# Performance work log

Hardware: AMD Instinct MI355X
Metric: run time of the kernel (lower is better)

Reference implementation:

```python
import jax, jax.numpy as jnp
import numpy as np

B, N, E, H, FF = 8, 1024, 512, 8, 2048
D = E // H
SCALE = D ** -0.5
EPS = 1e-5


def _layernorm(x, g, b):
    mu = jnp.mean(x, axis=-1, keepdims=True)
    var = jnp.mean((x - mu) ** 2, axis=-1, keepdims=True)
    return (x - mu) * jax.lax.rsqrt(var + EPS) * g + b


def setup_inputs() -> dict:
    key = jax.random.key(0)
    ks = jax.random.split(key, 16)
    s = lambda fan_in: 1.0 / np.sqrt(fan_in)
    inp = {"x": jax.random.normal(ks[0], (B, N, E), jnp.float32)}
    # attention projections, stored as [in, out] so y = x @ W + b
    inp["Wq"] = jax.random.uniform(ks[1], (E, E), jnp.float32, -s(E), s(E))
    inp["bq"] = jnp.zeros((E,), jnp.float32)
    inp["Wk"] = jax.random.uniform(ks[2], (E, E), jnp.float32, -s(E), s(E))
    inp["bk"] = jnp.zeros((E,), jnp.float32)
    inp["Wv"] = jax.random.uniform(ks[3], (E, E), jnp.float32, -s(E), s(E))
    inp["bv"] = jnp.zeros((E,), jnp.float32)
    inp["Wo"] = jax.random.uniform(ks[4], (E, E), jnp.float32, -s(E), s(E))
    inp["bo"] = jnp.zeros((E,), jnp.float32)
    # layernorms
    inp["g1"] = jnp.ones((E,), jnp.float32)
    inp["b1"] = jnp.zeros((E,), jnp.float32)
    inp["g2"] = jnp.ones((E,), jnp.float32)
    inp["b2"] = jnp.zeros((E,), jnp.float32)
    # feed-forward
    inp["W1"] = jax.random.uniform(ks[5], (E, FF), jnp.float32, -s(E), s(E))
    inp["bf1"] = jnp.zeros((FF,), jnp.float32)
    inp["W2"] = jax.random.uniform(ks[6], (FF, E), jnp.float32, -s(FF), s(FF))
    inp["bf2"] = jnp.zeros((E,), jnp.float32)
    return inp


def reference(x, Wq, bq, Wk, bk, Wv, bv, Wo, bo, g1, b1, g2, b2, W1, bf1, W2, bf2):
    # --- multi-head self-attention (equivalent to the edge scatter-softmax:
    # softmax over all source nodes j for each target node i) ---
    q = (x @ Wq + bq).reshape(B, N, H, D)
    k = (x @ Wk + bk).reshape(B, N, H, D)
    v = (x @ Wv + bv).reshape(B, N, H, D)
    scores = jnp.einsum("bnhd,bmhd->bhnm", q, k) * SCALE  # [B,H,N,N]
    attn = jax.nn.softmax(scores, axis=-1)
    ctx = jnp.einsum("bhnm,bmhd->bnhd", attn, v).reshape(B, N, E)
    attn_out = ctx @ Wo + bo
    # --- residual + norm1 ---
    h1 = _layernorm(x + attn_out, g1, b1)
    # --- FFN: linear -> relu -> linear ---
    ffn = jax.nn.relu(h1 @ W1 + bf1) @ W2 + bf2
    # --- residual + norm2 ---
    return _layernorm(h1 + ffn, g2, b2)
```

## Files before the change

kernel.cpp:

```cpp
#include <hip/hip_runtime.h>
#include <cstdint>
#include <cstddef>

typedef unsigned short u16;
typedef __attribute__((ext_vector_type(8))) short bf16x8;
typedef __attribute__((ext_vector_type(4))) float f32x4;
typedef __attribute__((ext_vector_type(16))) float f32x16;

#define EPI_F32 0
#define EPI_BF16_RELU 1
#define EPI_QKV 2
#define EPI_PART 3

#define QSCALE 0.18033688011112042f

__device__ __forceinline__ u16 f2bf(float f) {
  uint32_t u = __float_as_uint(f);
  return (u16)((u + 0x7FFFu + ((u >> 16) & 1u)) >> 16);
}

__device__ __forceinline__ uint32_t cvt_pk_bf16(float lo, float hi) {
  uint32_t r;
  asm("v_cvt_pk_bf16_f32 %0, %1, %2" : "=v"(r) : "v"(lo), "v"(hi));
  return r;
}

__device__ __forceinline__ float fexp2(float x) { return __builtin_amdgcn_exp2f(x); }

__device__ __forceinline__ void gload_lds16(const void* g, void* l) {
  __builtin_amdgcn_global_load_lds((const __attribute__((address_space(1))) void*)g,
                                   (__attribute__((address_space(3))) void*)l, 16, 0, 0);
}

__device__ __forceinline__ void tcvt_tile(const float* __restrict__ W,
                                          u16* __restrict__ Wt, int K, int N,
                                          int bx, int by, float (*tl)[33], int t) {
  const int kr0 = by * 32, nc0 = bx * 32;
  const int r = t >> 3, cq = (t & 7) * 4;
  float4 v = *(const float4*)&W[(size_t)(kr0 + r) * N + nc0 + cq];
  tl[r][cq + 0] = v.x; tl[r][cq + 1] = v.y; tl[r][cq + 2] = v.z; tl[r][cq + 3] = v.w;
  __syncthreads();
  union { u16 u[4]; uint2 q; } pk;
#pragma unroll
  for (int j = 0; j < 4; ++j) pk.u[j] = f2bf(tl[cq + j][r]);
  *(uint2*)&Wt[(size_t)(nc0 + r) * K + kr0 + cq] = pk.q;
}

__global__ __launch_bounds__(256) void prep_kernel(
    const float* __restrict__ x, u16* __restrict__ xb,
    const float* __restrict__ Wq, const float* __restrict__ Wk,
    const float* __restrict__ Wv, const float* __restrict__ Wo,
    u16* __restrict__ Wqkvt, u16* __restrict__ Wot,
    const float* __restrict__ W1, u16* __restrict__ W1t,
    const float* __restrict__ W2, u16* __restrict__ W2t,
    const float* __restrict__ bq, const float* __restrict__ bk,
    const float* __restrict__ bv, float* __restrict__ bqkv) {
  __shared__ float tl[32][33];
  const int b = blockIdx.x, t = threadIdx.x;
  if (b < 2048) {
    const int i = b * 256 + t;
    const float4* p = (const float4*)x + (size_t)i * 2;
    float4 a = p[0], c = p[1];
    union { u16 u[8]; uint4 q; } pk;
    pk.u[0] = f2bf(a.x); pk.u[1] = f2bf(a.y); pk.u[2] = f2bf(a.z); pk.u[3] = f2bf(a.w);
    pk.u[4] = f2bf(c.x); pk.u[5] = f2bf(c.y); pk.u[6] = f2bf(c.z); pk.u[7] = f2bf(c.w);
    ((uint4*)xb)[i] = pk.q;
  } else if (b < 3072) {
    const int u = b - 2048, z = u >> 8, s = u & 255;
    const float* W = z == 0 ? Wq : (z == 1 ? Wk : (z == 2 ? Wv : Wo));
    u16* Wt = z < 3 ? Wqkvt + z * 262144 : Wot;
    tcvt_tile(W, Wt, 512, 512, s & 15, s >> 4, tl, t);
  } else if (b < 4096) {
    const int u = b - 3072;
    tcvt_tile(W1, W1t, 512, 2048, u % 64, u / 64, tl, t);
  } else if (b < 5120) {
    const int u = b - 4096;
    tcvt_tile(W2, W2t, 2048, 512, u % 16, u / 16, tl, t);
  } else {
    const int i = (b - 5120) * 256 + t;
    if (i < 1536) bqkv[i] = i < 512 ? bq[i] : (i < 1024 ? bk[i - 512] : bv[i - 1024]);
  }
}

template<int BM, int BN, int WM, int WN, int EPI, int SPLIT>
__global__ __launch_bounds__(256, 2) void gemm2_kernel(
    const u16* __restrict__ A, const u16* __restrict__ Bt,
    const float* __restrict__ bias, void* __restrict__ out,
    int M, int N, int K) {
  constexpr int NWN = BN / WN;
  constexpr int MI = WM / 16, NI = WN / 16;
  __shared__ u16 As[2][BM * 64];
  __shared__ u16 Bs[2][BN * 64];
  const int tid = threadIdx.x, lane = tid & 63, wave = tid >> 6;
  const int m0 = blockIdx.y * BM, n0 = blockIdx.x * BN;
  const int wm = wave / NWN, wn = wave % NWN;
  const int g = lane >> 4, lr = lane & 15;
  const int srow = tid >> 3, sslot = tid & 7;

#define STAGE2(buf, k0) do {                                                        \
    _Pragma("unroll")                                                               \
    for (int i_ = 0; i_ < BM / 32; ++i_) {                                          \
      const int r_ = i_ * 32 + srow;                                                \
      gload_lds16(A + (size_t)(m0 + r_) * K + (k0) + ((sslot ^ (r_ & 7)) << 3),     \
                  &As[buf][i_ * 2048 + tid * 8]);                                   \
    }                                                                               \
    _Pragma("unroll")                                                               \
    for (int i_ = 0; i_ < BN / 32; ++i_) {                                          \
      const int r_ = i_ * 32 + srow;                                                \
      gload_lds16(Bt + (size_t)(n0 + r_) * K + (k0) + ((sslot ^ (r_ & 7)) << 3),    \
                  &Bs[buf][i_ * 2048 + tid * 8]);                                   \
    }                                                                               \
  } while (0)

  f32x4 acc[MI][NI] = {};
  const int kBeg = (SPLIT > 1) ? blockIdx.z * (K / SPLIT) : 0;
  const int NT = ((SPLIT > 1) ? K / SPLIT : K) >> 6;

  STAGE2(0, kBeg);
  STAGE2(1, kBeg + 64);
  asm volatile("s_waitcnt vmcnt(8)" ::: "memory");
  __builtin_amdgcn_s_barrier();
  asm volatile("" ::: "memory");

  for (int t = 0; t < NT; ++t) {
    const int cur = t & 1;
    bf16x8 af[MI][2], bf[NI][2];
#pragma unroll
    for (int step = 0; step < 2; ++step) {
#pragma unroll
      for (int mi = 0; mi < MI; ++mi) {
        const int r = wm * WM + mi * 16 + lr;
        af[mi][step] = *(const bf16x8*)&As[cur][r * 64 + ((((step << 2) + g) ^ (r & 7)) << 3)];
      }
#pragma unroll
      for (int ni = 0; ni < NI; ++ni) {
        const int r = wn * WN + ni * 16 + lr;
        bf[ni][step] = *(const bf16x8*)&Bs[cur][r * 64 + ((((step << 2) + g) ^ (r & 7)) << 3)];
      }
    }
    __builtin_amdgcn_s_setprio(1);
#pragma unroll
    for (int step = 0; step < 2; ++step)
#pragma unroll
      for (int mi = 0; mi < MI; ++mi)
#pragma unroll
        for (int ni = 0; ni < NI; ++ni)
          acc[mi][ni] = __builtin_amdgcn_mfma_f32_16x16x32_bf16(af[mi][step], bf[ni][step],
                                                                acc[mi][ni], 0, 0, 0);
    __builtin_amdgcn_s_setprio(0);
    asm volatile("s_waitcnt lgkmcnt(0)" ::: "memory");
    __builtin_amdgcn_sched_barrier(0);
    __builtin_amdgcn_s_barrier();
    asm volatile("" ::: "memory");
    if (t + 2 < NT) {
      STAGE2(cur, kBeg + (t + 2) * 64);
      asm volatile("s_waitcnt vmcnt(8)" ::: "memory");
    } else {
      asm volatile("s_waitcnt vmcnt(0)" ::: "memory");
    }
    __builtin_amdgcn_s_barrier();
    asm volatile("" ::: "memory");
  }
#undef STAGE2

#pragma unroll
  for (int mi = 0; mi < MI; ++mi) {
#pragma unroll
    for (int ni = 0; ni < NI; ++ni) {
      const int col = n0 + wn * WN + ni * 16 + lr;
      const float bv = (EPI == EPI_PART) ? 0.f : bias[col];
      f32x4 v = acc[mi][ni];
#pragma unroll
      for (int r = 0; r < 4; ++r) {
        const int row = m0 + wm * WM + mi * 16 + g * 4 + r;
        const float y = v[r] + bv;
        if (EPI == EPI_F32) {
          ((float*)out)[(size_t)row * N + col] = y;
        } else if (EPI == EPI_PART) {
          ((float*)out)[(size_t)blockIdx.z * M * N + (size_t)row * N + col] = y;
        } else if (EPI == EPI_BF16_RELU) {
          ((u16*)out)[(size_t)row * N + col] = f2bf(fmaxf(y, 0.f));
        } else {
          u16* qb = (u16*)out;
          const int sec = col >> 9, cs = col & 511;
          const int b = row >> 10, tt = row & 1023, h = cs >> 6, d = cs & 63;
          if (sec == 0)
            qb[((size_t)((b * 8 + h) * 1024 + tt)) * 64 + d] = f2bf(y * QSCALE);
          else if (sec == 1)
            qb[4194304 + ((size_t)((b * 8 + h) * 1024 + tt)) * 64 + d] = f2bf(y);
          else
            qb[8388608 + ((size_t)((b * 8 + h) * 64 + d)) * 1024 + tt] = f2bf(y);
        }
      }
    }
  }
}

template<int BM, int BN, int WM, int WN, int EPI, int SPLIT>
__global__ __launch_bounds__(256) void gemm_kernel(
    const u16* __restrict__ A, const u16* __restrict__ Bt,
    const float* __restrict__ bias, void* __restrict__ out,
    int M, int N, int K) {
  constexpr int NWN = BN / WN;
  constexpr int MI = WM / 16, NI = WN / 16;
  __shared__ u16 As[BM * 32];
  __shared__ u16 Bs[BN * 32];
  const int tid = threadIdx.x;
  const int lane = tid & 63;
  const int wave = tid >> 6;
  const int m0 = blockIdx.y * BM;
  const int n0 = blockIdx.x * BN;
  const int wm = wave / NWN, wn = wave % NWN;
  const int g = lane >> 4, lr = lane & 15;
  const int srow = lane >> 2, scol = (lane & 3) * 8;

  f32x4 acc[MI][NI] = {};

  const int kBeg = (SPLIT > 1) ? blockIdx.z * (K / SPLIT) : 0;
  const int kEnd = (SPLIT > 1) ? kBeg + (K / SPLIT) : K;
  for (int k0 = kBeg; k0 < kEnd; k0 += 32) {
#pragma unroll
    for (int ch = wave; ch < BM / 16; ch += 4)
      gload_lds16(A + (size_t)(m0 + ch * 16 + srow) * K + k0 + scol, &As[ch * 512]);
#pragma unroll
    for (int ch = wave; ch < BN / 16; ch += 4)
      gload_lds16(Bt + (size_t)(n0 + ch * 16 + srow) * K + k0 + scol, &Bs[ch * 512]);
    __syncthreads();
    bf16x8 a[MI], b[NI];
#pragma unroll
    for (int mi = 0; mi < MI; ++mi) a[mi] = *(const bf16x8*)&As[(wm * WM + mi * 16 + lr) * 32 + g * 8];
#pragma unroll
    for (int ni = 0; ni < NI; ++ni) b[ni] = *(const bf16x8*)&Bs[(wn * WN + ni * 16 + lr) * 32 + g * 8];
#pragma unroll
    for (int mi = 0; mi < MI; ++mi)
#pragma unroll
      for (int ni = 0; ni < NI; ++ni)
        acc[mi][ni] = __builtin_amdgcn_mfma_f32_16x16x32_bf16(a[mi], b[ni], acc[mi][ni], 0, 0, 0);
    __syncthreads();
  }

#pragma unroll
  for (int mi = 0; mi < MI; ++mi) {
#pragma unroll
    for (int ni = 0; ni < NI; ++ni) {
      const int col = n0 + wn * WN + ni * 16 + lr;
      const float bv = (EPI == EPI_PART) ? 0.f : bias[col];
      f32x4 v = acc[mi][ni];
#pragma unroll
      for (int r = 0; r < 4; ++r) {
        const int row = m0 + wm * WM + mi * 16 + g * 4 + r;
        const float y = v[r] + bv;
        if (EPI == EPI_F32) {
          ((float*)out)[(size_t)row * N + col] = y;
        } else if (EPI == EPI_PART) {
          ((float*)out)[(size_t)blockIdx.z * M * N + (size_t)row * N + col] = y;
        } else if (EPI == EPI_BF16_RELU) {
          ((u16*)out)[(size_t)row * N + col] = f2bf(fmaxf(y, 0.f));
        }
      }
    }
  }
}

__global__ __launch_bounds__(256, 2) void attn4_kernel(
    const u16* __restrict__ Q, const u16* __restrict__ K,
    const u16* __restrict__ Vt, u16* __restrict__ ctx) {
  __shared__ u16 smem[16384];
  const int tid = threadIdx.x, lane = tid & 63, w = tid >> 6;
  const int bh = blockIdx.x >> 3, qb = blockIdx.x & 7;
  const int c = lane & 31, g = lane >> 5;
  const int q0 = qb * 128 + w * 32;

  const u16* Qp = Q + ((size_t)bh * 1024 + q0 + c) * 64 + g * 8;
  const bf16x8 qf0 = *(const bf16x8*)(Qp);
  const bf16x8 qf1 = *(const bf16x8*)(Qp + 16);
  const bf16x8 qf2 = *(const bf16x8*)(Qp + 32);
  const bf16x8 qf3 = *(const bf16x8*)(Qp + 48);

  const u16* Kbase = K + (size_t)bh * 65536;
  const u16* Vbase = Vt + (size_t)bh * 65536;

  const int r0 = w * 16 + (lane >> 3), r1 = r0 + 8;
  const int cg0 = ((lane & 7) ^ (r0 & 7)) << 3;
  const int cg1 = ((lane & 7) ^ (r1 & 7)) << 3;

#define STAGE(buf, key0) do {                                                       \
    gload_lds16(Kbase + (size_t)((key0) + r0) * 64 + cg0, &smem[(buf)*4096 + w*1024]);       \
    gload_lds16(Kbase + (size_t)((key0) + r1) * 64 + cg1, &smem[(buf)*4096 + w*1024 + 512]); \
    gload_lds16(Vbase + (size_t)r0 * 1024 + (key0) + cg0, &smem[8192 + (buf)*4096 + w*1024]);\
    gload_lds16(Vbase + (size_t)r1 * 1024 + (key0) + cg1, &smem[8192 + (buf)*4096 + w*1024 + 512]); \
  } while (0)

  const int cs = c & 7;
  const int ro0 = c * 64, ro1 = (32 + c) * 64;
#define KS(buf, ro, cg) (*(const bf16x8*)&smem[(buf)*4096 + (ro) + ((((cg)) ^ cs) << 3)])
#define VS(buf, ro, cg) (*(const bf16x8*)&smem[8192 + (buf)*4096 + (ro) + ((((cg)) ^ cs) << 3)])

  f32x16 cacc[2] = {};
  float mrun = -1e30f, lrun = 0.f;

  STAGE(0, 0);
  __syncthreads();

  for (int kt = 0; kt < 16; ++kt) {
    const int buf = kt & 1;
    if (kt < 15) STAGE(buf ^ 1, (kt + 1) * 64);

    const bf16x8 kf0 = KS(buf, ro0, g),     kf1 = KS(buf, ro0, 2 + g);
    const bf16x8 kf2 = KS(buf, ro0, 4 + g), kf3 = KS(buf, ro0, 6 + g);
    const bf16x8 kf4 = KS(buf, ro1, g),     kf5 = KS(buf, ro1, 2 + g);
    const bf16x8 kf6 = KS(buf, ro1, 4 + g), kf7 = KS(buf, ro1, 6 + g);

    f32x16 sa = {}, sb = {};
    sa = __builtin_amdgcn_mfma_f32_32x32x16_bf16(kf0, qf0, sa, 0, 0, 0);
    sb = __builtin_amdgcn_mfma_f32_32x32x16_bf16(kf4, qf0, sb, 0, 0, 0);
    sa = __builtin_amdgcn_mfma_f32_32x32x16_bf16(kf1, qf1, sa, 0, 0, 0);
    sb = __builtin_amdgcn_mfma_f32_32x32x16_bf16(kf5, qf1, sb, 0, 0, 0);
    sa = __builtin_amdgcn_mfma_f32_32x32x16_bf16(kf2, qf2, sa, 0, 0, 0);
    sb = __builtin_amdgcn_mfma_f32_32x32x16_bf16(kf6, qf2, sb, 0, 0, 0);
    sa = __builtin_amdgcn_mfma_f32_32x32x16_bf16(kf3, qf3, sa, 0, 0, 0);
    sb = __builtin_amdgcn_mfma_f32_32x32x16_bf16(kf7, qf3, sb, 0, 0, 0);

    float tm[16];
#pragma unroll
    for (int r = 0; r < 16; ++r) tm[r] = fmaxf(sa[r], sb[r]);
#pragma unroll
    for (int st = 8; st >= 1; st >>= 1)
#pragma unroll
      for (int r = 0; r < st; ++r) tm[r] = fmaxf(tm[r], tm[r + st]);
    const float mt = fmaxf(tm[0], __shfl_xor(tm[0], 32));
    if (!__all(mt <= mrun)) {
      const float mnew = fmaxf(mrun, mt);
      const float al = fexp2(mrun - mnew);
#pragma unroll
      for (int r = 0; r < 16; ++r) { cacc[0][r] *= al; cacc[1][r] *= al; }
      lrun *= al;
      mrun = mnew;
    }
    float pa[16], pb[16];
#pragma unroll
    for (int r = 0; r < 16; ++r) pa[r] = fexp2(sa[r] - mrun);
#pragma unroll
    for (int r = 0; r < 16; ++r) pb[r] = fexp2(sb[r] - mrun);
    float ts[16];
#pragma unroll
    for (int r = 0; r < 16; ++r) ts[r] = pa[r] + pb[r];
#pragma unroll
    for (int st = 8; st >= 1; st >>= 1)
#pragma unroll
      for (int r = 0; r < st; ++r) ts[r] += ts[r + st];
    lrun += ts[0] + __shfl_xor(ts[0], 32);

    uint32_t wda[8], pwa[8], wdb[8], pwb[8];
#pragma unroll
    for (int i = 0; i < 8; ++i) wda[i] = cvt_pk_bf16(pa[2 * i], pa[2 * i + 1]);
#pragma unroll
    for (int i = 0; i < 8; ++i) wdb[i] = cvt_pk_bf16(pb[2 * i], pb[2 * i + 1]);
#pragma unroll
    for (int i = 0; i < 8; ++i) pwa[i] = __shfl_xor((int)wda[i], 32);
#pragma unroll
    for (int i = 0; i < 8; ++i) pwb[i] = __shfl_xor((int)wdb[i], 32);
    union { uint32_t u[4]; bf16x8 v; } b0a, b1a, b0b, b1b;
    const bool glo = (g == 0);
    b0a.u[0] = glo ? wda[0] : pwa[2]; b0a.u[1] = glo ? wda[1] : pwa[3];
    b0a.u[2] = glo ? pwa[0] : wda[2]; b0a.u[3] = glo ? pwa[1] : wda[3];
    b1a.u[0] = glo ? wda[4] : pwa[6]; b1a.u[1] = glo ? wda[5] : pwa[7];
    b1a.u[2] = glo ? pwa[4] : wda[6]; b1a.u[3] = glo ? pwa[5] : wda[7];
    b0b.u[0] = glo ? wdb[0] : pwb[2]; b0b.u[1] = glo ? wdb[1] : pwb[3];
    b0b.u[2] = glo ? pwb[0] : wdb[2]; b0b.u[3] = glo ? pwb[1] : wdb[3];
    b1b.u[0] = glo ? wdb[4] : pwb[6]; b1b.u[1] = glo ? wdb[5] : pwb[7];
    b1b.u[2] = glo ? pwb[4] : wdb[6]; b1b.u[3] = glo ? pwb[5] : wdb[7];

    const bf16x8 va00 = VS(buf, ro0, g),     va01 = VS(buf, ro0, 2 + g);
    const bf16x8 vb00 = VS(buf, ro0, 4 + g), vb01 = VS(buf, ro0, 6 + g);
    const bf16x8 va10 = VS(buf, ro1, g),     va11 = VS(buf, ro1, 2 + g);
    const bf16x8 vb10 = VS(buf, ro1, 4 + g), vb11 = VS(buf, ro1, 6 + g);

    cacc[0] = __builtin_amdgcn_mfma_f32_32x32x16_bf16(va00, b0a.v, cacc[0], 0, 0, 0);
    cacc[1] = __builtin_amdgcn_mfma_f32_32x32x16_bf16(va10, b0a.v, cacc[1], 0, 0, 0);
    cacc[0] = __builtin_amdgcn_mfma_f32_32x32x16_bf16(va01, b1a.v, cacc[0], 0, 0, 0);
    cacc[1] = __builtin_amdgcn_mfma_f32_32x32x16_bf16(va11, b1a.v, cacc[1], 0, 0, 0);
    cacc[0] = __builtin_amdgcn_mfma_f32_32x32x16_bf16(vb00, b0b.v, cacc[0], 0, 0, 0);
    cacc[1] = __builtin_amdgcn_mfma_f32_32x32x16_bf16(vb10, b0b.v, cacc[1], 0, 0, 0);
    cacc[0] = __builtin_amdgcn_mfma_f32_32x32x16_bf16(vb01, b1b.v, cacc[0], 0, 0, 0);
    cacc[1] = __builtin_amdgcn_mfma_f32_32x32x16_bf16(vb11, b1b.v, cacc[1], 0, 0, 0);

    __syncthreads();
  }

  const float inv = 1.0f / lrun;
  u16* tw = &smem[w * 2048];
#pragma unroll
  for (int h2 = 0; h2 < 2; ++h2) {
#pragma unroll
    for (int rq = 0; rq < 4; ++rq) {
      const u16 x0 = f2bf(cacc[h2][4 * rq + 0] * inv);
      const u16 x1 = f2bf(cacc[h2][4 * rq + 1] * inv);
      const u16 x2 = f2bf(cacc[h2][4 * rq + 2] * inv);
      const u16 x3 = f2bf(cacc[h2][4 * rq + 3] * inv);
      uint2 val;
      val.x = (uint32_t)x0 | ((uint32_t)x1 << 16);
      val.y = (uint32_t)x2 | ((uint32_t)x3 << 16);
      const int chunk = h2 * 4 + rq;
      *(uint2*)&tw[c * 64 + ((chunk ^ (c & 7)) * 8) + 4 * g] = val;
    }
  }
  __syncthreads();
  const int b_ = bh >> 3, h_ = bh & 7;
#pragma unroll
  for (int t = 0; t < 4; ++t) {
    const int lcg = t * 256 + tid;
    const int wv = lcg >> 8, rem = lcg & 255;
    const int q = rem >> 3, cg = rem & 7;
    const uint4 val = *(const uint4*)&smem[wv * 2048 + q * 64 + ((cg ^ (q & 7)) * 8)];
    const int grow = qb * 128 + wv * 32 + q;
    *(uint4*)&ctx[((size_t)(b_ * 1024 + grow)) * 512 + h_ * 64 + cg * 8] = val;
  }
#undef STAGE
#undef KS
#undef VS
}

template<bool ABF16>
__global__ __launch_bounds__(256) void lnc_kernel(
    const void* __restrict__ Av, const float* __restrict__ P0,
    const float* __restrict__ P1, const float* __restrict__ pb,
    const float* __restrict__ gw, const float* __restrict__ bw,
    float* __restrict__ outF, u16* __restrict__ outB) {
  const int lane = threadIdx.x & 63, wave = threadIdx.x >> 6;
  const int row = blockIdx.x * 4 + wave;
  float a[8];
  if (ABF16) {
    const uint4 q = ((const uint4*)((const u16*)Av + (size_t)row * 512))[lane];
    const u16* pu = (const u16*)&q;
#pragma unroll
    for (int j = 0; j < 8; ++j) a[j] = __uint_as_float((uint32_t)pu[j] << 16);
  } else {
    const float4* a4 = (const float4*)((const float*)Av + (size_t)row * 512);
    const float4 x0 = a4[lane * 2], x1 = a4[lane * 2 + 1];
    a[0] = x0.x; a[1] = x0.y; a[2] = x0.z; a[3] = x0.w;
    a[4] = x1.x; a[5] = x1.y; a[6] = x1.z; a[7] = x1.w;
  }
  const float4* p04 = (const float4*)(P0 + (size_t)row * 512);
  const float4* p14 = (const float4*)(P1 + (size_t)row * 512);
  const float4 q00 = p04[lane * 2], q01 = p04[lane * 2 + 1];
  const float4 q10 = p14[lane * 2], q11 = p14[lane * 2 + 1];
  const float4 e0 = ((const float4*)pb)[lane * 2], e1 = ((const float4*)pb)[lane * 2 + 1];
  float v[8] = {a[0] + q00.x + q10.x + e0.x, a[1] + q00.y + q10.y + e0.y,
                a[2] + q00.z + q10.z + e0.z, a[3] + q00.w + q10.w + e0.w,
                a[4] + q01.x + q11.x + e1.x, a[5] + q01.y + q11.y + e1.y,
                a[6] + q01.z + q11.z + e1.z, a[7] + q01.w + q11.w + e1.w};
  float s = 0.f;
#pragma unroll
  for (int j = 0; j < 8; ++j) s += v[j];
#pragma unroll
  for (int off = 32; off >= 1; off >>= 1) s += __shfl_xor(s, off);
  const float mu = s * (1.f / 512.f);
  float vs = 0.f;
#pragma unroll
  for (int j = 0; j < 8; ++j) { const float d = v[j] - mu; vs += d * d; }
#pragma unroll
  for (int off = 32; off >= 1; off >>= 1) vs += __shfl_xor(vs, off);
  const float rstd = rsqrtf(vs * (1.f / 512.f) + 1e-5f);
  const float4 gA = ((const float4*)gw)[lane * 2], gB = ((const float4*)gw)[lane * 2 + 1];
  const float4 bA = ((const float4*)bw)[lane * 2], bB = ((const float4*)bw)[lane * 2 + 1];
  const float og[8] = {gA.x, gA.y, gA.z, gA.w, gB.x, gB.y, gB.z, gB.w};
  const float ob[8] = {bA.x, bA.y, bA.z, bA.w, bB.x, bB.y, bB.z, bB.w};
  float o[8];
#pragma unroll
  for (int j = 0; j < 8; ++j) o[j] = (v[j] - mu) * rstd * og[j] + ob[j];
  if (outF) {
    float4 w0 = {o[0], o[1], o[2], o[3]}, w1 = {o[4], o[5], o[6], o[7]};
    ((float4*)(outF + (size_t)row * 512))[lane * 2] = w0;
    ((float4*)(outF + (size_t)row * 512))[lane * 2 + 1] = w1;
  }
  if (outB) {
    union { u16 u[8]; uint4 q; } pk;
#pragma unroll
    for (int j = 0; j < 8; ++j) pk.u[j] = f2bf(o[j]);
    ((uint4*)(outB + (size_t)row * 512))[lane] = pk.q;
  }
}

extern "C" void kernel_launch(void* const* d_in, const int* in_sizes, int n_in,
                              void* d_out, int out_size, void* d_ws, size_t ws_size,
                              hipStream_t stream) {
  const float* x   = (const float*)d_in[0];
  const float* Wq  = (const float*)d_in[1];
  const float* bq  = (const float*)d_in[2];
  const float* Wk  = (const float*)d_in[3];
  const float* bk  = (const float*)d_in[4];
  const float* Wv  = (const float*)d_in[5];
  const float* bv  = (const float*)d_in[6];
  const float* Wo  = (const float*)d_in[7];
  const float* bo  = (const float*)d_in[8];
  const float* g1  = (const float*)d_in[9];
  const float* b1  = (const float*)d_in[10];
  const float* g2  = (const float*)d_in[11];
  const float* b2  = (const float*)d_in[12];
  const float* W1  = (const float*)d_in[13];
  const float* bf1 = (const float*)d_in[14];
  const float* W2  = (const float*)d_in[15];
  const float* bf2 = (const float*)d_in[16];

  char* ws = (char*)d_ws;
  u16*   xb    = (u16*)(ws + 0);
  u16*   Wqkvt = (u16*)(ws + 8388608);
  u16*   Wot   = (u16*)(ws + 9961472);
  u16*   W1t   = (u16*)(ws + 10485760);
  u16*   W2t   = (u16*)(ws + 12582912);
  u16*   Qb    = (u16*)(ws + 14680064);
  u16*   ctx   = (u16*)(ws + 39845888);
  float* P0    = (float*)(ws + 48234496);
  u16*   h1b   = (u16*)(ws + 81788928);
  u16*   mid   = (u16*)(ws + 14680064);
  float* bqkv  = (float*)(ws + 39845888);

  prep_kernel<<<5126, 256, 0, stream>>>(x, xb, Wq, Wk, Wv, Wo, Wqkvt, Wot,
                                        W1, W1t, W2, W2t, bq, bk, bv, bqkv);

  gemm2_kernel<128, 128, 64, 64, EPI_QKV, 1><<<dim3(12, 64), 256, 0, stream>>>(
      xb, Wqkvt, bqkv, Qb, 8192, 1536, 512);

  attn4_kernel<<<512, 256, 0, stream>>>(Qb, Qb + 4194304, Qb + 8388608, ctx);

  gemm_kernel<64, 128, 64, 32, EPI_PART, 2><<<dim3(4, 128, 2), 256, 0, stream>>>(
      ctx, Wot, nullptr, P0, 8192, 512, 512);
  lnc_kernel<true><<<2048, 256, 0, stream>>>(xb, P0, P0 + 4194304, bo, g1, b1,
                                             nullptr, h1b);

  gemm2_kernel<128, 128, 64, 64, EPI_BF16_RELU, 1><<<dim3(16, 64), 256, 0, stream>>>(
      h1b, W1t, bf1, mid, 8192, 2048, 512);

  gemm_kernel<64, 128, 64, 32, EPI_PART, 2><<<dim3(4, 128, 2), 256, 0, stream>>>(
      mid, W2t, nullptr, P0, 8192, 512, 2048);
  lnc_kernel<true><<<2048, 256, 0, stream>>>(h1b, P0, P0 + 4194304, bf2, g2, b2,
                                             (float*)d_out, nullptr);
}
```

Measured before the change: 264.6 us.

## Replace GEMM kernels with barrier-free per-wave LDS staging GEMM

```diff
diff --git a/kernel.cpp b/kernel.cpp
--- a/kernel.cpp
+++ b/kernel.cpp
@@ -82,97 +82,74 @@
   }
 }
 
-template<int BM, int BN, int WM, int WN, int EPI, int SPLIT>
-__global__ __launch_bounds__(256, 2) void gemm2_kernel(
+template<int EPI, int SPLIT>
+__global__ __launch_bounds__(256, 2) void gemm3_kernel(
     const u16* __restrict__ A, const u16* __restrict__ Bt,
     const float* __restrict__ bias, void* __restrict__ out,
     int M, int N, int K) {
-  constexpr int NWN = BN / WN;
-  constexpr int MI = WM / 16, NI = WN / 16;
-  __shared__ u16 As[2][BM * 64];
-  __shared__ u16 Bs[2][BN * 64];
+  __shared__ u16 lds[32768];
   const int tid = threadIdx.x, lane = tid & 63, wave = tid >> 6;
-  const int m0 = blockIdx.y * BM, n0 = blockIdx.x * BN;
-  const int wm = wave / NWN, wn = wave % NWN;
+  const int m0 = blockIdx.y * 128, n0 = blockIdx.x * 128;
+  const int wm = wave >> 1, wn = wave & 1;
   const int g = lane >> 4, lr = lane & 15;
-  const int srow = tid >> 3, sslot = tid & 7;
-
-#define STAGE2(buf, k0) do {                                                        \
-    _Pragma("unroll")                                                               \
-    for (int i_ = 0; i_ < BM / 32; ++i_) {                                          \
-      const int r_ = i_ * 32 + srow;                                                \
-      gload_lds16(A + (size_t)(m0 + r_) * K + (k0) + ((sslot ^ (r_ & 7)) << 3),     \
-                  &As[buf][i_ * 2048 + tid * 8]);                                   \
-    }                                                                               \
-    _Pragma("unroll")                                                               \
-    for (int i_ = 0; i_ < BN / 32; ++i_) {                                          \
-      const int r_ = i_ * 32 + srow;                                                \
-      gload_lds16(Bt + (size_t)(n0 + r_) * K + (k0) + ((sslot ^ (r_ & 7)) << 3),    \
-                  &Bs[buf][i_ * 2048 + tid * 8]);                                   \
-    }                                                                               \
+  const int rs = lr & 3;
+  u16* wl = &lds[wave * 8192];
+
+  const int soff = (((lane & 3) ^ ((lane >> 2) & 3)) << 3);
+  const u16* Ab = A + (size_t)(m0 + wm * 64 + (lane >> 2)) * K + soff;
+  const u16* Bb = Bt + (size_t)(n0 + wn * 64 + (lane >> 2)) * K + soff;
+
+#define ST3(buf, k0) do {                                                  \
+    _Pragma("unroll") for (int i_ = 0; i_ < 4; ++i_)                       \
+      gload_lds16(Ab + (size_t)(i_ * 16) * K + (k0),                       \
+                  &wl[(buf) * 2048 + i_ * 512 + lane * 8]);                \
+    _Pragma("unroll") for (int i_ = 0; i_ < 4; ++i_)                       \
+      gload_lds16(Bb + (size_t)(i_ * 16) * K + (k0),                       \
+                  &wl[4096 + (buf) * 2048 + i_ * 512 + lane * 8]);         \
   } while (0)
 
-  f32x4 acc[MI][NI] = {};
+  f32x4 acc[4][4] = {};
   const int kBeg = (SPLIT > 1) ? blockIdx.z * (K / SPLIT) : 0;
-  const int NT = ((SPLIT > 1) ? K / SPLIT : K) >> 6;
-
-  STAGE2(0, kBeg);
-  STAGE2(1, kBeg + 64);
-  asm volatile("s_waitcnt vmcnt(8)" ::: "memory");
-  __builtin_amdgcn_s_barrier();
-  asm volatile("" ::: "memory");
+  const int NT = ((SPLIT > 1) ? K / SPLIT : K) >> 5;
+
+  ST3(0, kBeg);
+  ST3(1, kBeg + 32);
 
   for (int t = 0; t < NT; ++t) {
-    const int cur = t & 1;
-    bf16x8 af[MI][2], bf[NI][2];
-#pragma unroll
-    for (int step = 0; step < 2; ++step) {
-#pragma unroll
-      for (int mi = 0; mi < MI; ++mi) {
-        const int r = wm * WM + mi * 16 + lr;
-        af[mi][step] = *(const bf16x8*)&As[cur][r * 64 + ((((step << 2) + g) ^ (r & 7)) << 3)];
-      }
-#pragma unroll
-      for (int ni = 0; ni < NI; ++ni) {
-        const int r = wn * WN + ni * 16 + lr;
-        bf[ni][step] = *(const bf16x8*)&Bs[cur][r * 64 + ((((step << 2) + g) ^ (r & 7)) << 3)];
-      }
-    }
-    __builtin_amdgcn_s_setprio(1);
-#pragma unroll
-    for (int step = 0; step < 2; ++step)
-#pragma unroll
-      for (int mi = 0; mi < MI; ++mi)
-#pragma unroll
-        for (int ni = 0; ni < NI; ++ni)
-          acc[mi][ni] = __builtin_amdgcn_mfma_f32_16x16x32_bf16(af[mi][step], bf[ni][step],
-                                                                acc[mi][ni], 0, 0, 0);
-    __builtin_amdgcn_s_setprio(0);
+    const int buf = t & 1;
+    if (t + 1 < NT) { asm volatile("s_waitcnt vmcnt(8)" ::: "memory"); }
+    else            { asm volatile("s_waitcnt vmcnt(0)" ::: "memory"); }
+    bf16x8 af[4], bfr[4];
+#pragma unroll
+    for (int mi = 0; mi < 4; ++mi)
+      af[mi] = *(const bf16x8*)&wl[buf * 2048 + (mi * 16 + lr) * 32 + ((g ^ rs) << 3)];
+#pragma unroll
+    for (int ni = 0; ni < 4; ++ni)
+      bfr[ni] = *(const bf16x8*)&wl[4096 + buf * 2048 + (ni * 16 + lr) * 32 + ((g ^ rs) << 3)];
     asm volatile("s_waitcnt lgkmcnt(0)" ::: "memory");
     __builtin_amdgcn_sched_barrier(0);
-    __builtin_amdgcn_s_barrier();
-    asm volatile("" ::: "memory");
-    if (t + 2 < NT) {
-      STAGE2(cur, kBeg + (t + 2) * 64);
-      asm volatile("s_waitcnt vmcnt(8)" ::: "memory");
-    } else {
-      asm volatile("s_waitcnt vmcnt(0)" ::: "memory");
-    }
-    __builtin_amdgcn_s_barrier();
-    asm volatile("" ::: "memory");
-  }
-#undef STAGE2
-
-#pragma unroll
-  for (int mi = 0; mi < MI; ++mi) {
-#pragma unroll
-    for (int ni = 0; ni < NI; ++ni) {
-      const int col = n0 + wn * WN + ni * 16 + lr;
+    if (t + 2 < NT) ST3(buf, kBeg + (t + 2) * 32);
+    __builtin_amdgcn_s_setprio(1);
+#pragma unroll
+    for (int mi = 0; mi < 4; ++mi)
+#pragma unroll
+      for (int ni = 0; ni < 4; ++ni)
+        acc[mi][ni] = __builtin_amdgcn_mfma_f32_16x16x32_bf16(af[mi], bfr[ni],
+                                                              acc[mi][ni], 0, 0, 0);
+    __builtin_amdgcn_s_setprio(0);
+  }
+#undef ST3
+
+#pragma unroll
+  for (int mi = 0; mi < 4; ++mi) {
+#pragma unroll
+    for (int ni = 0; ni < 4; ++ni) {
+      const int col = n0 + wn * 64 + ni * 16 + lr;
       const float bv = (EPI == EPI_PART) ? 0.f : bias[col];
       f32x4 v = acc[mi][ni];
 #pragma unroll
       for (int r = 0; r < 4; ++r) {
-        const int row = m0 + wm * WM + mi * 16 + g * 4 + r;
+        const int row = m0 + wm * 64 + mi * 16 + g * 4 + r;
         const float y = v[r] + bv;
         if (EPI == EPI_F32) {
           ((float*)out)[(size_t)row * N + col] = y;
@@ -196,72 +173,6 @@
   }
 }
 
-template<int BM, int BN, int WM, int WN, int EPI, int SPLIT>
-__global__ __launch_bounds__(256) void gemm_kernel(
-    const u16* __restrict__ A, const u16* __restrict__ Bt,
-    const float* __restrict__ bias, void* __restrict__ out,
-    int M, int N, int K) {
-  constexpr int NWN = BN / WN;
-  constexpr int MI = WM / 16, NI = WN / 16;
-  __shared__ u16 As[BM * 32];
-  __shared__ u16 Bs[BN * 32];
-  const int tid = threadIdx.x;
-  const int lane = tid & 63;
-  const int wave = tid >> 6;
-  const int m0 = blockIdx.y * BM;
-  const int n0 = blockIdx.x * BN;
-  const int wm = wave / NWN, wn = wave % NWN;
-  const int g = lane >> 4, lr = lane & 15;
-  const int srow = lane >> 2, scol = (lane & 3) * 8;
-
-  f32x4 acc[MI][NI] = {};
-
-  const int kBeg = (SPLIT > 1) ? blockIdx.z * (K / SPLIT) : 0;
-  const int kEnd = (SPLIT > 1) ? kBeg + (K / SPLIT) : K;
-  for (int k0 = kBeg; k0 < kEnd; k0 += 32) {
-#pragma unroll
-    for (int ch = wave; ch < BM / 16; ch += 4)
-      gload_lds16(A + (size_t)(m0 + ch * 16 + srow) * K + k0 + scol, &As[ch * 512]);
-#pragma unroll
-    for (int ch = wave; ch < BN / 16; ch += 4)
-      gload_lds16(Bt + (size_t)(n0 + ch * 16 + srow) * K + k0 + scol, &Bs[ch * 512]);
-    __syncthreads();
-    bf16x8 a[MI], b[NI];
-#pragma unroll
-    for (int mi = 0; mi < MI; ++mi) a[mi] = *(const bf16x8*)&As[(wm * WM + mi * 16 + lr) * 32 + g * 8];
-#pragma unroll
-    for (int ni = 0; ni < NI; ++ni) b[ni] = *(const bf16x8*)&Bs[(wn * WN + ni * 16 + lr) * 32 + g * 8];
-#pragma unroll
-    for (int mi = 0; mi < MI; ++mi)
-#pragma unroll
-      for (int ni = 0; ni < NI; ++ni)
-        acc[mi][ni] = __builtin_amdgcn_mfma_f32_16x16x32_bf16(a[mi], b[ni], acc[mi][ni], 0, 0, 0);
-    __syncthreads();
-  }
-
-#pragma unroll
-  for (int mi = 0; mi < MI; ++mi) {
-#pragma unroll
-    for (int ni = 0; ni < NI; ++ni) {
-      const int col = n0 + wn * WN + ni * 16 + lr;
-      const float bv = (EPI == EPI_PART) ? 0.f : bias[col];
-      f32x4 v = acc[mi][ni];
-#pragma unroll
-      for (int r = 0; r < 4; ++r) {
-        const int row = m0 + wm * WM + mi * 16 + g * 4 + r;
-        const float y = v[r] + bv;
-        if (EPI == EPI_F32) {
-          ((float*)out)[(size_t)row * N + col] = y;
-        } else if (EPI == EPI_PART) {
-          ((float*)out)[(size_t)blockIdx.z * M * N + (size_t)row * N + col] = y;
-        } else if (EPI == EPI_BF16_RELU) {
-          ((u16*)out)[(size_t)row * N + col] = f2bf(fmaxf(y, 0.f));
-        }
-      }
-    }
-  }
-}
-
 __global__ __launch_bounds__(256, 2) void attn4_kernel(
     const u16* __restrict__ Q, const u16* __restrict__ K,
     const u16* __restrict__ Vt, u16* __restrict__ ctx) {
@@ -519,20 +430,20 @@
   prep_kernel<<<5126, 256, 0, stream>>>(x, xb, Wq, Wk, Wv, Wo, Wqkvt, Wot,
                                         W1, W1t, W2, W2t, bq, bk, bv, bqkv);
 
-  gemm2_kernel<128, 128, 64, 64, EPI_QKV, 1><<<dim3(12, 64), 256, 0, stream>>>(
+  gemm3_kernel<EPI_QKV, 1><<<dim3(12, 64), 256, 0, stream>>>(
       xb, Wqkvt, bqkv, Qb, 8192, 1536, 512);
 
   attn4_kernel<<<512, 256, 0, stream>>>(Qb, Qb + 4194304, Qb + 8388608, ctx);
 
-  gemm_kernel<64, 128, 64, 32, EPI_PART, 2><<<dim3(4, 128, 2), 256, 0, stream>>>(
+  gemm3_kernel<EPI_PART, 2><<<dim3(4, 64, 2), 256, 0, stream>>>(
       ctx, Wot, nullptr, P0, 8192, 512, 512);
   lnc_kernel<true><<<2048, 256, 0, stream>>>(xb, P0, P0 + 4194304, bo, g1, b1,
                                              nullptr, h1b);
 
-  gemm2_kernel<128, 128, 64, 64, EPI_BF16_RELU, 1><<<dim3(16, 64), 256, 0, stream>>>(
+  gemm3_kernel<EPI_BF16_RELU, 1><<<dim3(16, 64), 256, 0, stream>>>(
       h1b, W1t, bf1, mid, 8192, 2048, 512);
 
-  gemm_kernel<64, 128, 64, 32, EPI_PART, 2><<<dim3(4, 128, 2), 256, 0, stream>>>(
+  gemm3_kernel<EPI_PART, 2><<<dim3(4, 64, 2), 256, 0, stream>>>(
       mid, W2t, nullptr, P0, 8192, 512, 2048);
   lnc_kernel<true><<<2048, 256, 0, stream>>>(h1b, P0, P0 + 4194304, bf2, g2, b2,
                                              (float*)d_out, nullptr);
```

After: 276.5 us. +4.5%, slower.

## Replace tiled GEMM with A-resident 32-row blocks streaming per-wave B tiles

Applied to the files above, without the earlier changes.

```diff
diff --git a/kernel.cpp b/kernel.cpp
--- a/kernel.cpp
+++ b/kernel.cpp
@@ -82,118 +82,105 @@
   }
 }
 
-template<int BM, int BN, int WM, int WN, int EPI, int SPLIT>
-__global__ __launch_bounds__(256, 2) void gemm2_kernel(
+template<int EPI>
+__global__ __launch_bounds__(256, 2) void gemm4_kernel(
     const u16* __restrict__ A, const u16* __restrict__ Bt,
     const float* __restrict__ bias, void* __restrict__ out,
     int M, int N, int K) {
-  constexpr int NWN = BN / WN;
-  constexpr int MI = WM / 16, NI = WN / 16;
-  __shared__ u16 As[2][BM * 64];
-  __shared__ u16 Bs[2][BN * 64];
+  __shared__ u16 lds[16384 + 4 * 3 * 2048];
   const int tid = threadIdx.x, lane = tid & 63, wave = tid >> 6;
-  const int m0 = blockIdx.y * BM, n0 = blockIdx.x * BN;
-  const int wm = wave / NWN, wn = wave % NWN;
+  const int m0 = blockIdx.x * 32;
   const int g = lane >> 4, lr = lane & 15;
-  const int srow = tid >> 3, sslot = tid & 7;
-
-#define STAGE2(buf, k0) do {                                                        \
-    _Pragma("unroll")                                                               \
-    for (int i_ = 0; i_ < BM / 32; ++i_) {                                          \
-      const int r_ = i_ * 32 + srow;                                                \
-      gload_lds16(A + (size_t)(m0 + r_) * K + (k0) + ((sslot ^ (r_ & 7)) << 3),     \
-                  &As[buf][i_ * 2048 + tid * 8]);                                   \
-    }                                                                               \
-    _Pragma("unroll")                                                               \
-    for (int i_ = 0; i_ < BN / 32; ++i_) {                                          \
-      const int r_ = i_ * 32 + srow;                                                \
-      gload_lds16(Bt + (size_t)(n0 + r_) * K + (k0) + ((sslot ^ (r_ & 7)) << 3),    \
-                  &Bs[buf][i_ * 2048 + tid * 8]);                                   \
-    }                                                                               \
+  u16* Bw = &lds[16384 + wave * 3 * 2048];
+  const int NTILE = N >> 8;
+
+#pragma unroll
+  for (int j = 0; j < 8; ++j) {
+    const int f = j * 256 + tid;
+    const int row = f >> 6, grp = f & 63;
+    const int sgrp = (grp & ~7) | ((grp & 7) ^ (row & 7));
+    gload_lds16(A + (size_t)(m0 + row) * K + sgrp * 8, &lds[f * 8]);
+  }
+
+  const int brow = lane >> 2, bk = lane & 3;
+#define STB(gsv) do {                                                        \
+    const int gs_ = (gsv);                                                   \
+    int nt_ = gs_ >> 4; if (nt_ > NTILE - 1) nt_ = NTILE - 1;                \
+    const int ks_ = gs_ & 15, buf_ = gs_ % 3;                                \
+    const u16* Bb_ = Bt + (size_t)(nt_ * 256 + wave * 64) * K + ks_ * 32;    \
+    _Pragma("unroll") for (int i_ = 0; i_ < 4; ++i_) {                       \
+      const int r_ = i_ * 16 + brow;                                         \
+      gload_lds16(Bb_ + (size_t)r_ * K + ((bk ^ (r_ & 3)) << 3),             \
+                  &Bw[buf_ * 2048 + i_ * 512 + lane * 8]);                   \
+    }                                                                        \
   } while (0)
 
-  f32x4 acc[MI][NI] = {};
-  const int kBeg = (SPLIT > 1) ? blockIdx.z * (K / SPLIT) : 0;
-  const int NT = ((SPLIT > 1) ? K / SPLIT : K) >> 6;
-
-  STAGE2(0, kBeg);
-  STAGE2(1, kBeg + 64);
-  asm volatile("s_waitcnt vmcnt(8)" ::: "memory");
-  __builtin_amdgcn_s_barrier();
-  asm volatile("" ::: "memory");
-
-  for (int t = 0; t < NT; ++t) {
-    const int cur = t & 1;
-    bf16x8 af[MI][2], bf[NI][2];
-#pragma unroll
-    for (int step = 0; step < 2; ++step) {
-#pragma unroll
-      for (int mi = 0; mi < MI; ++mi) {
-        const int r = wm * WM + mi * 16 + lr;
-        af[mi][step] = *(const bf16x8*)&As[cur][r * 64 + ((((step << 2) + g) ^ (r & 7)) << 3)];
+  STB(0); STB(1); STB(2);
+  asm volatile("s_waitcnt vmcnt(12)" ::: "memory");
+  __syncthreads();
+
+  for (int nt = 0; nt < NTILE; ++nt) {
+    f32x4 acc[2][4] = {};
+    for (int ks = 0; ks < 16; ++ks) {
+      const int gs = nt * 16 + ks;
+      const int buf = gs % 3;
+      asm volatile("s_waitcnt vmcnt(8)" ::: "memory");
+      bf16x8 af[2], bfr[4];
+#pragma unroll
+      for (int mi = 0; mi < 2; ++mi) {
+        const int row = mi * 16 + lr;
+        const int G = ks * 4 + g;
+        const int slot = (G & ~7) | ((G & 7) ^ (row & 7));
+        af[mi] = *(const bf16x8*)&lds[row * 512 + slot * 8];
       }
 #pragma unroll
-      for (int ni = 0; ni < NI; ++ni) {
-        const int r = wn * WN + ni * 16 + lr;
-        bf[ni][step] = *(const bf16x8*)&Bs[cur][r * 64 + ((((step << 2) + g) ^ (r & 7)) << 3)];
+      for (int ni = 0; ni < 4; ++ni) {
+        const int r = ni * 16 + lr;
+        bfr[ni] = *(const bf16x8*)&Bw[buf * 2048 + r * 32 + ((g ^ (r & 3)) << 3)];
       }
+      asm volatile("s_waitcnt lgkmcnt(0)" ::: "memory");
+      __builtin_amdgcn_sched_barrier(0);
+      STB(gs + 3);
+      __builtin_amdgcn_s_setprio(1);
+#pragma unroll
+      for (int mi = 0; mi < 2; ++mi)
+#pragma unroll
+        for (int ni = 0; ni < 4; ++ni)
+          acc[mi][ni] = __builtin_amdgcn_mfma_f32_16x16x32_bf16(af[mi], bfr[ni],
+                                                                acc[mi][ni], 0, 0, 0);
+      __builtin_amdgcn_s_setprio(0);
     }
-    __builtin_amdgcn_s_setprio(1);
-#pragma unroll
-    for (int step = 0; step < 2; ++step)
-#pragma unroll
-      for (int mi = 0; mi < MI; ++mi)
-#pragma unroll
-        for (int ni = 0; ni < NI; ++ni)
-          acc[mi][ni] = __builtin_amdgcn_mfma_f32_16x16x32_bf16(af[mi][step], bf[ni][step],
-                                                                acc[mi][ni], 0, 0, 0);
-    __builtin_amdgcn_s_setprio(0);
-    asm volatile("s_waitcnt lgkmcnt(0)" ::: "memory");
-    __builtin_amdgcn_sched_barrier(0);
-    __builtin_amdgcn_s_barrier();
-    asm volatile("" ::: "memory");
-    if (t + 2 < NT) {
-      STAGE2(cur, kBeg + (t + 2) * 64);
-      asm volatile("s_waitcnt vmcnt(8)" ::: "memory");
-    } else {
-      asm volatile("s_waitcnt vmcnt(0)" ::: "memory");
-    }
-    __builtin_amdgcn_s_barrier();
-    asm volatile("" ::: "memory");
-  }
-#undef STAGE2
-
-#pragma unroll
-  for (int mi = 0; mi < MI; ++mi) {
-#pragma unroll
-    for (int ni = 0; ni < NI; ++ni) {
-      const int col = n0 + wn * WN + ni * 16 + lr;
-      const float bv = (EPI == EPI_PART) ? 0.f : bias[col];
-      f32x4 v = acc[mi][ni];
-#pragma unroll
-      for (int r = 0; r < 4; ++r) {
-        const int row = m0 + wm * WM + mi * 16 + g * 4 + r;
-        const float y = v[r] + bv;
-        if (EPI == EPI_F32) {
-          ((float*)out)[(size_t)row * N + col] = y;
-        } else if (EPI == EPI_PART) {
-          ((float*)out)[(size_t)blockIdx.z * M * N + (size_t)row * N + col] = y;
-        } else if (EPI == EPI_BF16_RELU) {
-          ((u16*)out)[(size_t)row * N + col] = f2bf(fmaxf(y, 0.f));
-        } else {
-          u16* qb = (u16*)out;
-          const int sec = col >> 9, cs = col & 511;
-          const int b = row >> 10, tt = row & 1023, h = cs >> 6, d = cs & 63;
-          if (sec == 0)
-            qb[((size_t)((b * 8 + h) * 1024 + tt)) * 64 + d] = f2bf(y * QSCALE);
-          else if (sec == 1)
-            qb[4194304 + ((size_t)((b * 8 + h) * 1024 + tt)) * 64 + d] = f2bf(y);
-          else
-            qb[8388608 + ((size_t)((b * 8 + h) * 64 + d)) * 1024 + tt] = f2bf(y);
+#pragma unroll
+    for (int mi = 0; mi < 2; ++mi) {
+#pragma unroll
+      for (int ni = 0; ni < 4; ++ni) {
+        const int col = nt * 256 + wave * 64 + ni * 16 + lr;
+        const float bv = bias[col];
+        f32x4 v = acc[mi][ni];
+#pragma unroll
+        for (int r = 0; r < 4; ++r) {
+          const int row = m0 + mi * 16 + g * 4 + r;
+          const float y = v[r] + bv;
+          if (EPI == EPI_F32) {
+            ((float*)out)[(size_t)row * N + col] = y;
+          } else if (EPI == EPI_BF16_RELU) {
+            ((u16*)out)[(size_t)row * N + col] = f2bf(fmaxf(y, 0.f));
+          } else {
+            u16* qb = (u16*)out;
+            const int sec = col >> 9, cs = col & 511;
+            const int b = row >> 10, tt = row & 1023, h = cs >> 6, d = cs & 63;
+            if (sec == 0)
+              qb[((size_t)((b * 8 + h) * 1024 + tt)) * 64 + d] = f2bf(y * QSCALE);
+            else if (sec == 1)
+              qb[4194304 + ((size_t)((b * 8 + h) * 1024 + tt)) * 64 + d] = f2bf(y);
+            else
+              qb[8388608 + ((size_t)((b * 8 + h) * 64 + d)) * 1024 + tt] = f2bf(y);
+          }
         }
       }
     }
   }
+#undef STB
 }
 
 template<int BM, int BN, int WM, int WN, int EPI, int SPLIT>
@@ -421,7 +408,7 @@
 #undef VS
 }
 
-template<bool ABF16>
+template<bool ABF16, bool TWOP>
 __global__ __launch_bounds__(256) void lnc_kernel(
     const void* __restrict__ Av, const float* __restrict__ P0,
     const float* __restrict__ P1, const float* __restrict__ pb,
@@ -442,14 +429,16 @@
     a[4] = x1.x; a[5] = x1.y; a[6] = x1.z; a[7] = x1.w;
   }
   const float4* p04 = (const float4*)(P0 + (size_t)row * 512);
-  const float4* p14 = (const float4*)(P1 + (size_t)row * 512);
   const float4 q00 = p04[lane * 2], q01 = p04[lane * 2 + 1];
-  const float4 q10 = p14[lane * 2], q11 = p14[lane * 2 + 1];
-  const float4 e0 = ((const float4*)pb)[lane * 2], e1 = ((const float4*)pb)[lane * 2 + 1];
-  float v[8] = {a[0] + q00.x + q10.x + e0.x, a[1] + q00.y + q10.y + e0.y,
-                a[2] + q00.z + q10.z + e0.z, a[3] + q00.w + q10.w + e0.w,
-                a[4] + q01.x + q11.x + e1.x, a[5] + q01.y + q11.y + e1.y,
-                a[6] + q01.z + q11.z + e1.z, a[7] + q01.w + q11.w + e1.w};
+  float v[8] = {a[0] + q00.x, a[1] + q00.y, a[2] + q00.z, a[3] + q00.w,
+                a[4] + q01.x, a[5] + q01.y, a[6] + q01.z, a[7] + q01.w};
+  if (TWOP) {
+    const float4* p14 = (const float4*)(P1 + (size_t)row * 512);
+    const float4 q10 = p14[lane * 2], q11 = p14[lane * 2 + 1];
+    const float4 e0 = ((const float4*)pb)[lane * 2], e1 = ((const float4*)pb)[lane * 2 + 1];
+    v[0] += q10.x + e0.x; v[1] += q10.y + e0.y; v[2] += q10.z + e0.z; v[3] += q10.w + e0.w;
+    v[4] += q11.x + e1.x; v[5] += q11.y + e1.y; v[6] += q11.z + e1.z; v[7] += q11.w + e1.w;
+  }
   float s = 0.f;
 #pragma unroll
   for (int j = 0; j < 8; ++j) s += v[j];
@@ -519,21 +508,21 @@
   prep_kernel<<<5126, 256, 0, stream>>>(x, xb, Wq, Wk, Wv, Wo, Wqkvt, Wot,
                                         W1, W1t, W2, W2t, bq, bk, bv, bqkv);
 
-  gemm2_kernel<128, 128, 64, 64, EPI_QKV, 1><<<dim3(12, 64), 256, 0, stream>>>(
+  gemm4_kernel<EPI_QKV><<<256, 256, 0, stream>>>(
       xb, Wqkvt, bqkv, Qb, 8192, 1536, 512);
 
   attn4_kernel<<<512, 256, 0, stream>>>(Qb, Qb + 4194304, Qb + 8388608, ctx);
 
-  gemm_kernel<64, 128, 64, 32, EPI_PART, 2><<<dim3(4, 128, 2), 256, 0, stream>>>(
-      ctx, Wot, nullptr, P0, 8192, 512, 512);
-  lnc_kernel<true><<<2048, 256, 0, stream>>>(xb, P0, P0 + 4194304, bo, g1, b1,
-                                             nullptr, h1b);
-
-  gemm2_kernel<128, 128, 64, 64, EPI_BF16_RELU, 1><<<dim3(16, 64), 256, 0, stream>>>(
+  gemm4_kernel<EPI_F32><<<256, 256, 0, stream>>>(
+      ctx, Wot, bo, P0, 8192, 512, 512);
+  lnc_kernel<true, false><<<2048, 256, 0, stream>>>(xb, P0, nullptr, nullptr,
+                                                    g1, b1, nullptr, h1b);
+
+  gemm4_kernel<EPI_BF16_RELU><<<256, 256, 0, stream>>>(
       h1b, W1t, bf1, mid, 8192, 2048, 512);
 
   gemm_kernel<64, 128, 64, 32, EPI_PART, 2><<<dim3(4, 128, 2), 256, 0, stream>>>(
       mid, W2t, nullptr, P0, 8192, 512, 2048);
-  lnc_kernel<true><<<2048, 256, 0, stream>>>(h1b, P0, P0 + 4194304, bf2, g2, b2,
-                                             (float*)d_out, nullptr);
-}
+  lnc_kernel<true, true><<<2048, 256, 0, stream>>>(h1b, P0, P0 + 4194304, bf2,
+                                                   g2, b2, (float*)d_out, nullptr);
+}
```

Result: slower. 287.5 us (+8.6%).
